# Optimization experiments

Hardware: AMD Instinct MI355X
Metric: run time of the kernel (lower is better)

Reference implementation:

```python
import jax, jax.numpy as jnp
import numpy as np

K = 20      # neighbors per node
D_T = 32    # timestep embedding dim

def _timestep_embedding(t, dim):
    half = dim // 2
    freqs = jnp.exp(-jnp.log(10000.0) * jnp.arange(half, dtype=jnp.float32) / (half - 1))
    args = t[:, None] * freqs[None, :]
    return jnp.concatenate([jnp.sin(args), jnp.cos(args)], axis=-1)

def _knn(pos, k):
    # pos: [N,3] -> (sources, targets): [N*k] edge index lists
    r2 = jnp.sum(pos * pos, axis=-1)
    d2 = r2[:, None] + r2[None, :] - 2.0 * (pos @ pos.T)   # [N,N] squared distances
    n = pos.shape[0]
    d2 = d2 + 1e10 * jnp.eye(n, dtype=pos.dtype)           # exclude self
    d2 = jax.lax.stop_gradient(d2)                         # indices only, no grad path
    _, idx = jax.lax.top_k(-d2, k)                         # [N,k]
    targets = jnp.repeat(jnp.arange(n), k)
    sources = idx.reshape(-1)
    return sources, targets

def _forward(z, t, conditioning, Wc1, bc1, Wc2, bc2, Wc3, bc3, We1, be1, We2, be2, Wn1, bn1, Wn2, bn2, alpha, beta):
    B, N, _ = z.shape
    pos, vel, massf = z[..., :3], z[..., 3:6], z[..., 6:]
    t = t * jnp.ones((B,), z.dtype)
    temb = _timestep_embedding(t, D_T)                     # [B,32]
    cond = jnp.concatenate([temb, conditioning], axis=1)   # [B,36]
    h = jax.nn.gelu(cond @ Wc1 + bc1)
    h = jax.nn.gelu(h @ Wc2 + bc2)
    cond = h @ Wc3 + bc3                                   # [B,36]
    fs = massf + cond[:, None, :]                          # scalar node feats [B,N,36]

    def single(pos_b, vel_b, fs_b):
        src, tgt = _knn(pos_b, K)
        rel = pos_b[src] - pos_b[tgt]                      # [E,3]
        r2 = jnp.sum(rel * rel, axis=-1, keepdims=True)
        vs, vt = vel_b[src], vel_b[tgt]
        # rotation-invariant edge features
        inv = jnp.concatenate([
            fs_b[src], fs_b[tgt], r2,
            jnp.sum(vs * vt, -1, keepdims=True),
            jnp.sum(vs * rel, -1, keepdims=True),
            jnp.sum(vt * rel, -1, keepdims=True),
        ], axis=-1)                                        # [E,76]
        e = jax.nn.gelu(inv @ We1 + be1) @ We2 + be2       # [E,4]
        logit, smsg, c_rel, c_vel = e[:, 0], e[:, 1], e[:, 2], e[:, 3]
        # segment softmax over incoming edges of each target node
        m = jax.ops.segment_max(logit, tgt, num_segments=N)
        a = jnp.exp(logit - m[tgt])
        denom = jax.ops.segment_sum(a, tgt, num_segments=N)
        w = a / denom[tgt]
        # equivariant vector messages, invariant scalar messages
        vmsg = w[:, None] * (c_rel[:, None] * rel + c_vel[:, None] * vs)
        vagg = jax.ops.segment_sum(vmsg, tgt, num_segments=N)              # [N,3]
        sagg = jax.ops.segment_sum(w * smsg, tgt, num_segments=N)[:, None]  # [N,1]
        hn = jax.nn.gelu(jnp.concatenate([fs_b, sagg], axis=-1) @ Wn1 + bn1)
        sout = hn @ Wn2 + bn2                              # [N,1] 0e output
        pos_out = pos_b + alpha * vagg                     # 1o
        feat_out = jnp.concatenate([beta * vagg, sout], axis=-1)  # 1o + 0e
        return jnp.concatenate([pos_out, feat_out], axis=-1)      # [N,7]

    h_all = jax.vmap(single)(pos, vel, fs)
    return z + h_all

def setup_inputs():
    key = jax.random.key(0)
    ks = jax.random.split(key, 10)
    B, N = 2, 8192
    d_cond = D_T + 4          # 36
    e_in = 2 * d_cond + 4     # 76
    e_hid, n_hid = 128, 64
    g = lambda i, shp: jax.random.normal(ks[i], shp, jnp.float32) * 0.05
    return {
        "z": jax.random.normal(ks[0], (B, N, 7), jnp.float32),
        "t": jax.random.uniform(ks[1], (B,), jnp.float32),
        "conditioning": jax.random.normal(ks[2], (B, 4), jnp.float32),
        "mask": jnp.ones((B, N), dtype=bool),
        "Wc1": g(3, (d_cond, 4 * d_cond)), "bc1": jnp.zeros((4 * d_cond,), jnp.float32),
        "Wc2": g(4, (4 * d_cond, 4 * d_cond)), "bc2": jnp.zeros((4 * d_cond,), jnp.float32),
        "Wc3": g(5, (4 * d_cond, d_cond)), "bc3": jnp.zeros((d_cond,), jnp.float32),
        "We1": g(6, (e_in, e_hid)), "be1": jnp.zeros((e_hid,), jnp.float32),
        "We2": g(7, (e_hid, 4)), "be2": jnp.zeros((4,), jnp.float32),
        "Wn1": g(8, (d_cond + 1, n_hid)), "bn1": jnp.zeros((n_hid,), jnp.float32),
        "Wn2": g(9, (n_hid, 1)), "bn2": jnp.zeros((1,), jnp.float32),
        "alpha": jnp.float32(0.1), "beta": jnp.float32(0.1),
    }

def reference(z, t, conditioning, mask, Wc1, bc1, Wc2, bc2, Wc3, bc3, We1, be1, We2, be2, Wn1, bn1, Wn2, bn2, alpha, beta):
    # mask is unused (module docstring: does not support masking)
    return _forward(z, t, conditioning, Wc1, bc1, Wc2, bc2, Wc3, bc3, We1, be1, We2, be2, Wn1, bn1, Wn2, bn2, alpha, beta)
```

## Files before the change

### kernel.cpp

```cpp
#include <hip/hip_runtime.h>
#include <math.h>

#define NB 8192
#define BATCH 2
#define KNN 20
#define BN (BATCH*NB)
#define NE (BN*KNN)
#define GT 16
#define NG 8
#define BIG 3.0e38f

__device__ __forceinline__ float gelu_f(float x){
    float x3 = x*x*x;
    float a = 0.7978845608028654f*(x + 0.044715f*x3);
    float e2 = __expf(2.0f*a);
    float th = 1.0f - __fdividef(2.0f, e2+1.0f);
    return 0.5f*x*(1.0f+th);
}

__global__ __launch_bounds__(256) void prepcond_kernel(const float* __restrict__ z,
        const float* __restrict__ t,
        const float* __restrict__ conditioning,
        const float* __restrict__ Wc1, const float* __restrict__ bc1,
        const float* __restrict__ Wc2, const float* __restrict__ bc2,
        const float* __restrict__ Wc3, const float* __restrict__ bc3,
        const float* __restrict__ We1, const float* __restrict__ be1,
        const float* __restrict__ We2,
        const float* __restrict__ Wn1, const float* __restrict__ bn1,
        float4* __restrict__ pos4, float4* __restrict__ vel4,
        float* __restrict__ consts, float* __restrict__ pack){
    int tid = threadIdx.x;
    int g = blockIdx.x*256 + tid;
    const float* zp = z + (size_t)g*7;
    float x = zp[0], y = zp[1], zz = zp[2];
    float r2 = x*x + y*y + zz*zz;
    pos4[g] = make_float4(x, y, zz, r2);
    vel4[g] = make_float4(zp[3], zp[4], zp[5], zp[6]);

    if (blockIdx.x >= BATCH) return;
    int b = blockIdx.x;
    __shared__ float ci[36];
    __shared__ float h1[144];
    __shared__ float h2[144];
    __shared__ float cnd[36];
    float tv = t[b];
    if (tid < 16){
        float f = expf(-9.210340371976184f * (float)tid / 15.0f);
        float a = tv*f;
        ci[tid]    = sinf(a);
        ci[16+tid] = cosf(a);
    }
    if (tid < 4) ci[32+tid] = conditioning[b*4+tid];
    __syncthreads();
    if (tid < 144){
        float acc = bc1[tid];
        #pragma unroll
        for (int c=0;c<36;c++) acc += ci[c]*Wc1[c*144+tid];
        h1[tid] = gelu_f(acc);
    }
    __syncthreads();
    if (tid < 144){
        float acc = bc2[tid];
        #pragma unroll 36
        for (int c=0;c<144;c++) acc += h1[c]*Wc2[c*144+tid];
        h2[tid] = gelu_f(acc);
    }
    __syncthreads();
    if (tid < 36){
        float acc = bc3[tid];
        #pragma unroll 36
        for (int c=0;c<144;c++) acc += h2[c]*Wc3[c*36+tid];
        cnd[tid] = acc;
    }
    __syncthreads();
    if (tid < 128){
        float accC = be1[tid], s1 = 0.f, s2 = 0.f;
        #pragma unroll
        for (int c=0;c<36;c++){
            float w1 = We1[c*128+tid];
            float w2 = We1[(36+c)*128+tid];
            accC += cnd[c]*(w1+w2);
            s1 += w1; s2 += w2;
        }
        consts[b*128+tid] = accC;
        pack[tid*12 + b] = accC;
        if (b==0){
            consts[256+tid] = s1; consts[384+tid] = s2;
            pack[tid*12+2] = s1;
            pack[tid*12+3] = s2;
            pack[tid*12+4] = We1[72*128+tid];
            pack[tid*12+5] = We1[73*128+tid];
            pack[tid*12+6] = We1[74*128+tid];
            pack[tid*12+7] = We1[75*128+tid];
            pack[tid*12+8]  = We2[tid*4+0];
            pack[tid*12+9]  = We2[tid*4+1];
            pack[tid*12+10] = We2[tid*4+2];
            pack[tid*12+11] = We2[tid*4+3];
        }
    }
    if (tid < 64){
        float accD = bn1[tid], t1 = 0.f;
        #pragma unroll
        for (int c=0;c<36;c++){
            float w = Wn1[c*64+tid];
            accD += cnd[c]*w;
            t1 += w;
        }
        consts[512 + b*64 + tid] = accD;
        if (b==0) consts[640+tid] = t1;
    }
}

__global__ __launch_bounds__(512, 4) void knn_kernel(const float4* __restrict__ pos4,
                                                     int* __restrict__ nbr){
    __shared__ float4 sPos[GT*64];
    __shared__ float2 sCand[32*64];
    int tid = threadIdx.x;
    int w = tid >> 6, lane = tid & 63;
    int n0g = blockIdx.x * 32;
    int b = n0g >> 13;
    int n0 = n0g & (NB-1);
    const float4* __restrict__ P = pos4 + b*NB;

    int nw = n0 + w*4;
    float nx[4], ny[4], nz[4], acc[4];
    #pragma unroll
    for (int k=0;k<4;k++){
        float4 p = P[nw+k];
        nx[k] = -2.0f*p.x; ny[k] = -2.0f*p.y; nz[k] = -2.0f*p.z;
        acc[k] = BIG;
    }
    int selfTile = n0 >> 6;
    int sl0 = (n0 & 63) + w*4;

    float4 pre0 = P[(w*2    )*64 + lane];
    float4 pre1 = P[(w*2 + 1)*64 + lane];
    for (int g=0; g<NG; ++g){
        __syncthreads();
        sPos[(w*2    )*64 + lane] = pre0;
        sPos[(w*2 + 1)*64 + lane] = pre1;
        if (g+1 < NG){
            pre0 = P[((g+1)*GT + w*2    )*64 + lane];
            pre1 = P[((g+1)*GT + w*2 + 1)*64 + lane];
        }
        __syncthreads();
        int tbase = g*GT;
        #pragma unroll
        for (int t=0;t<GT;t++){
            float4 q = sPos[t*64 + lane];
            if (tbase + t != selfTile){
                #pragma unroll
                for (int k=0;k<4;k++){
                    float d2 = fmaf(nx[k],q.x, fmaf(ny[k],q.y, fmaf(nz[k],q.z, q.w)));
                    acc[k] = fminf(acc[k], d2);
                }
            } else {
                #pragma unroll
                for (int k=0;k<4;k++){
                    float d2 = fmaf(nx[k],q.x, fmaf(ny[k],q.y, fmaf(nz[k],q.z, q.w)));
                    if (lane == sl0 + k) d2 = BIG;
                    acc[k] = fminf(acc[k], d2);
                }
            }
        }
    }

    float T[4];
    #pragma unroll
    for (int k=0;k<4;k++){
        float v = acc[k];
        #pragma unroll
        for (int K=2; K<=64; K<<=1){
            #pragma unroll
            for (int j=K>>1; j>0; j>>=1){
                float o = __shfl_xor(v, j);
                bool keepmin = (((lane & j) == 0) == ((lane & K) == 0));
                float mn = fminf(v,o), mx = fmaxf(v,o);
                v = keepmin ? mn : mx;
            }
        }
        T[k] = __shfl(v, 19);
    }

    int cnt[4];
    #pragma unroll
    for (int k=0;k<4;k++) cnt[k] = 0;
    unsigned long long lt = (1ull << lane) - 1ull;

    pre0 = P[(w*2    )*64 + lane];
    pre1 = P[(w*2 + 1)*64 + lane];
    for (int g=0; g<NG; ++g){
        __syncthreads();
        sPos[(w*2    )*64 + lane] = pre0;
        sPos[(w*2 + 1)*64 + lane] = pre1;
        if (g+1 < NG){
            pre0 = P[((g+1)*GT + w*2    )*64 + lane];
            pre1 = P[((g+1)*GT + w*2 + 1)*64 + lane];
        }
        __syncthreads();
        int tbase = g*GT;
        #pragma unroll 4
        for (int t=0;t<GT;t++){
            int tile = tbase + t;
            float4 q = sPos[t*64 + lane];
            int j = (tile<<6) + lane;
            bool selft = (tile == selfTile);
            #pragma unroll
            for (int k=0;k<4;k++){
                float d2 = fmaf(nx[k],q.x, fmaf(ny[k],q.y, fmaf(nz[k],q.z, q.w)));
                bool hit = (d2 <= T[k]);
                if (selft && (lane == sl0 + k)) hit = false;
                unsigned long long m = __ballot(hit);
                if (m){
                    if (hit){
                        int off = cnt[k] + (int)__popcll(m & lt);
                        if (off < 64)
                            sCand[(w*4+k)*64 + off] = make_float2(d2, __int_as_float(j));
                    }
                    cnt[k] += (int)__popcll(m);
                }
            }
        }
    }

    #pragma unroll
    for (int k=0;k<4;k++){
        int m = cnt[k]; if (m > 64) m = 64;
        float d; int idx;
        if (lane < m){
            float2 e = sCand[(w*4+k)*64 + lane];
            d = e.x; idx = __float_as_int(e.y);
        } else { d = BIG; idx = 0x7f000000 + lane; }
        #pragma unroll
        for (int K=2; K<=64; K<<=1){
            #pragma unroll
            for (int j=K>>1; j>0; j>>=1){
                float od = __shfl_xor(d, j);
                int   oi = __shfl_xor(idx, j);
                bool pless = (od < d) || (od == d && oi < idx);
                bool keepmin = (((lane & j) == 0) == ((lane & K) == 0));
                if (pless == keepmin){ d = od; idx = oi; }
            }
        }
        if (lane < KNN) nbr[(size_t)(n0g + w*4 + k)*KNN + lane] = idx;
    }
}

__global__ __launch_bounds__(320) void edgenode_kernel(const float4* __restrict__ pos4,
        const float4* __restrict__ vel4,
        const int* __restrict__ nbr,
        const float* __restrict__ pack,
        const float* __restrict__ consts,
        const float* __restrict__ Wn1,
        const float* __restrict__ Wn2,
        const float* __restrict__ be2,
        const float* __restrict__ bn2,
        const float* __restrict__ alpha_p,
        const float* __restrict__ beta_p,
        const float* __restrict__ z,
        float* __restrict__ out){
    __shared__ float4 sP[384];
    __shared__ float sLg[320], sSm[320], sUx[320], sUy[320], sUz[320];
    __shared__ float sD[64], sT1[64], sW36[64], sWo[64];
    __shared__ float sMf[16];
    __shared__ float4 sAgg[16];
    __shared__ float sPart[320];

    int tid = threadIdx.x;
    bool bb = (blockIdx.x >= 512);
    for (int k=tid; k<384; k+=320) sP[k] = ((const float4*)pack)[k];
    if (tid < 64){
        sD[tid]   = consts[512 + (bb?64:0) + tid];
        sT1[tid]  = consts[640+tid];
        sW36[tid] = Wn1[36*64+tid];
        sWo[tid]  = Wn2[tid];
    }

    int e = blockIdx.x*320 + tid;
    int i = e / KNN;
    int ln = tid / KNN;
    int r  = tid - ln*KNN;
    int bbase = bb ? NB : 0;
    int s = nbr[e];
    float4 ps = pos4[bbase + s], pt = pos4[i];
    float4 vs = vel4[bbase + s], vt = vel4[i];
    if (r == 0) sMf[ln] = vt.w;

    float rx = ps.x - pt.x, ry = ps.y - pt.y, rz = ps.z - pt.z;
    float r2  = rx*rx + ry*ry + rz*rz;
    float vv  = vs.x*vt.x + vs.y*vt.y + vs.z*vt.z;
    float vsr = vs.x*rx + vs.y*ry + vs.z*rz;
    float vtr = vt.x*rx + vt.y*ry + vt.z*rz;
    float mfs = vs.w, mft = vt.w;
    __syncthreads();

    float a0 = be2[0], a1 = be2[1], a2 = be2[2], a3 = be2[3];
    #pragma unroll 4
    for (int h=0; h<128; h++){
        float4 A  = sP[h*3];
        float4 Bv = sP[h*3+1];
        float4 C  = sP[h*3+2];
        float base = bb ? A.y : A.x;
        float x = base + mfs*A.z + mft*A.w + r2*Bv.x + vv*Bv.y + vsr*Bv.z + vtr*Bv.w;
        float gx = gelu_f(x);
        a0 += gx*C.x; a1 += gx*C.y; a2 += gx*C.z; a3 += gx*C.w;
    }
    sLg[tid] = a0;
    sSm[tid] = a1;
    sUx[tid] = a2*rx + a3*vs.x;
    sUy[tid] = a2*ry + a3*vs.y;
    sUz[tid] = a2*rz + a3*vs.z;
    __syncthreads();

    if (tid < 16){
        int base = tid*KNN;
        float m = -BIG;
        #pragma unroll
        for (int q=0;q<KNN;q++) m = fmaxf(m, sLg[base+q]);
        float den=0.f, wx=0.f, wy=0.f, wz=0.f, wsm=0.f;
        #pragma unroll
        for (int q=0;q<KNN;q++){
            float a = __expf(sLg[base+q]-m);
            den += a;
            wsm += a*sSm[base+q];
            wx  += a*sUx[base+q];
            wy  += a*sUy[base+q];
            wz  += a*sUz[base+q];
        }
        float inv = __fdividef(1.0f, den);
        sAgg[tid] = make_float4(wx*inv, wy*inv, wz*inv, wsm*inv);
    }
    __syncthreads();

    {
        float mf = sMf[ln];
        float sg = sAgg[ln].w;
        float part = 0.f;
        #pragma unroll
        for (int h=r; h<64; h+=KNN){
            float x = sD[h] + mf*sT1[h] + sg*sW36[h];
            part += gelu_f(x)*sWo[h];
        }
        sPart[tid] = part;
    }
    __syncthreads();

    if (tid < 16){
        float sout = bn2[0];
        #pragma unroll
        for (int q=0;q<KNN;q++) sout += sPart[tid*KNN+q];
        int node = blockIdx.x*16 + tid;
        float alpha = alpha_p[0], beta = beta_p[0];
        float4 ag = sAgg[tid];
        const float* zp = z + (size_t)node*7;
        float* op = out + (size_t)node*7;
        op[0] = zp[0]*2.0f + alpha*ag.x;
        op[1] = zp[1]*2.0f + alpha*ag.y;
        op[2] = zp[2]*2.0f + alpha*ag.z;
        op[3] = zp[3] + beta*ag.x;
        op[4] = zp[4] + beta*ag.y;
        op[5] = zp[5] + beta*ag.z;
        op[6] = zp[6] + sout;
    }
}

extern "C" void kernel_launch(void* const* d_in, const int* in_sizes, int n_in,
                              void* d_out, int out_size, void* d_ws, size_t ws_size,
                              hipStream_t stream) {
    const float* z    = (const float*)d_in[0];
    const float* t    = (const float*)d_in[1];
    const float* cond = (const float*)d_in[2];
    const float* Wc1  = (const float*)d_in[4];
    const float* bc1  = (const float*)d_in[5];
    const float* Wc2  = (const float*)d_in[6];
    const float* bc2  = (const float*)d_in[7];
    const float* Wc3  = (const float*)d_in[8];
    const float* bc3  = (const float*)d_in[9];
    const float* We1  = (const float*)d_in[10];
    const float* be1  = (const float*)d_in[11];
    const float* We2  = (const float*)d_in[12];
    const float* be2  = (const float*)d_in[13];
    const float* Wn1  = (const float*)d_in[14];
    const float* bn1  = (const float*)d_in[15];
    const float* Wn2  = (const float*)d_in[16];
    const float* bn2  = (const float*)d_in[17];
    const float* alp  = (const float*)d_in[18];
    const float* bet  = (const float*)d_in[19];
    float* out = (float*)d_out;

    char* ws = (char*)d_ws;
    float4* pos4   = (float4*)(ws);
    float4* vel4   = (float4*)(ws + 262144);
    float*  consts = (float*)(ws + 524288);
    float*  pack   = (float*)(ws + 528384);
    int*    nbr    = (int*)(ws + 534528);

    prepcond_kernel<<<dim3(BN/256), dim3(256), 0, stream>>>(z, t, cond,
        Wc1, bc1, Wc2, bc2, Wc3, bc3, We1, be1, We2, Wn1, bn1,
        pos4, vel4, consts, pack);
    knn_kernel<<<dim3(BN/32), dim3(512), 0, stream>>>(pos4, nbr);
    edgenode_kernel<<<dim3(BN/16), dim3(320), 0, stream>>>(pos4, vel4, nbr, pack, consts,
        Wn1, Wn2, be2, bn2, alp, bet, z, out);
}
```

Before: 201.5 us.

## Process two edges per thread in edgenode kernel and simplify GELU formula

Each thread in the edge/node kernel now handles two edges (32 nodes per block instead of 16), so each shared-memory weight load in the 128-wide hidden loop is reused for two edges. The block count halves and the batch split moves to block 256. GELU's tanh approximation is rewritten algebraically as x/(1+exp(-2a)), which saves a few instructions per evaluation. The trade-off is higher register pressure, more shared memory per block and fewer blocks.

```diff
diff --git a/kernel.cpp b/kernel.cpp
--- a/kernel.cpp
+++ b/kernel.cpp
@@ -11,11 +11,10 @@
 #define BIG 3.0e38f
 
 __device__ __forceinline__ float gelu_f(float x){
-    float x3 = x*x*x;
-    float a = 0.7978845608028654f*(x + 0.044715f*x3);
-    float e2 = __expf(2.0f*a);
-    float th = 1.0f - __fdividef(2.0f, e2+1.0f);
-    return 0.5f*x*(1.0f+th);
+    float t = x*x;
+    float m = x*fmaf(t, -0.0713548163f, -1.5957691216f);
+    float e = __expf(m);
+    return __fdividef(x, 1.0f + e);
 }
 
 __global__ __launch_bounds__(256) void prepcond_kernel(const float* __restrict__ z,
@@ -260,14 +259,14 @@
         const float* __restrict__ z,
         float* __restrict__ out){
     __shared__ float4 sP[384];
-    __shared__ float sLg[320], sSm[320], sUx[320], sUy[320], sUz[320];
+    __shared__ float sLg[640], sSm[640], sUx[640], sUy[640], sUz[640];
     __shared__ float sD[64], sT1[64], sW36[64], sWo[64];
-    __shared__ float sMf[16];
-    __shared__ float4 sAgg[16];
-    __shared__ float sPart[320];
+    __shared__ float sMf[32];
+    __shared__ float4 sAgg[32];
+    __shared__ float sPart[640];
 
     int tid = threadIdx.x;
-    bool bb = (blockIdx.x >= 512);
+    bool bb = (blockIdx.x >= 256);
     for (int k=tid; k<384; k+=320) sP[k] = ((const float4*)pack)[k];
     if (tid < 64){
         sD[tid]   = consts[512 + (bb?64:0) + tid];
@@ -276,43 +275,58 @@
         sWo[tid]  = Wn2[tid];
     }
 
-    int e = blockIdx.x*320 + tid;
-    int i = e / KNN;
-    int ln = tid / KNN;
-    int r  = tid - ln*KNN;
+    int e0 = blockIdx.x*640 + tid;
+    int e1 = e0 + 320;
+    int i0 = e0 / KNN;
+    int i1 = i0 + 16;
+    int ln0 = tid / KNN;
+    int r  = tid - ln0*KNN;
     int bbase = bb ? NB : 0;
-    int s = nbr[e];
-    float4 ps = pos4[bbase + s], pt = pos4[i];
-    float4 vs = vel4[bbase + s], vt = vel4[i];
-    if (r == 0) sMf[ln] = vt.w;
-
-    float rx = ps.x - pt.x, ry = ps.y - pt.y, rz = ps.z - pt.z;
-    float r2  = rx*rx + ry*ry + rz*rz;
-    float vv  = vs.x*vt.x + vs.y*vt.y + vs.z*vt.z;
-    float vsr = vs.x*rx + vs.y*ry + vs.z*rz;
-    float vtr = vt.x*rx + vt.y*ry + vt.z*rz;
-    float mfs = vs.w, mft = vt.w;
-    __syncthreads();
-
-    float a0 = be2[0], a1 = be2[1], a2 = be2[2], a3 = be2[3];
-    #pragma unroll 4
+    int s0 = nbr[e0], s1 = nbr[e1];
+    float4 ps0 = pos4[bbase + s0], pt0 = pos4[i0];
+    float4 vs0 = vel4[bbase + s0], vt0 = vel4[i0];
+    float4 ps1 = pos4[bbase + s1], pt1 = pos4[i1];
+    float4 vs1 = vel4[bbase + s1], vt1 = vel4[i1];
+    if (r == 0){ sMf[ln0] = vt0.w; sMf[ln0+16] = vt1.w; }
+
+    float rx0 = ps0.x - pt0.x, ry0 = ps0.y - pt0.y, rz0 = ps0.z - pt0.z;
+    float r20  = rx0*rx0 + ry0*ry0 + rz0*rz0;
+    float vv0  = vs0.x*vt0.x + vs0.y*vt0.y + vs0.z*vt0.z;
+    float vsr0 = vs0.x*rx0 + vs0.y*ry0 + vs0.z*rz0;
+    float vtr0 = vt0.x*rx0 + vt0.y*ry0 + vt0.z*rz0;
+    float mfs0 = vs0.w, mft0 = vt0.w;
+
+    float rx1 = ps1.x - pt1.x, ry1 = ps1.y - pt1.y, rz1 = ps1.z - pt1.z;
+    float r21  = rx1*rx1 + ry1*ry1 + rz1*rz1;
+    float vv1  = vs1.x*vt1.x + vs1.y*vt1.y + vs1.z*vt1.z;
+    float vsr1 = vs1.x*rx1 + vs1.y*ry1 + vs1.z*rz1;
+    float vtr1 = vt1.x*rx1 + vt1.y*ry1 + vt1.z*rz1;
+    float mfs1 = vs1.w, mft1 = vt1.w;
+    __syncthreads();
+
+    float a00 = be2[0], a10 = be2[1], a20 = be2[2], a30 = be2[3];
+    float a01 = a00, a11 = a10, a21 = a20, a31 = a30;
+    #pragma unroll 2
     for (int h=0; h<128; h++){
         float4 A  = sP[h*3];
         float4 Bv = sP[h*3+1];
         float4 C  = sP[h*3+2];
         float base = bb ? A.y : A.x;
-        float x = base + mfs*A.z + mft*A.w + r2*Bv.x + vv*Bv.y + vsr*Bv.z + vtr*Bv.w;
-        float gx = gelu_f(x);
-        a0 += gx*C.x; a1 += gx*C.y; a2 += gx*C.z; a3 += gx*C.w;
-    }
-    sLg[tid] = a0;
-    sSm[tid] = a1;
-    sUx[tid] = a2*rx + a3*vs.x;
-    sUy[tid] = a2*ry + a3*vs.y;
-    sUz[tid] = a2*rz + a3*vs.z;
-    __syncthreads();
-
-    if (tid < 16){
+        float x0 = base + mfs0*A.z + mft0*A.w + r20*Bv.x + vv0*Bv.y + vsr0*Bv.z + vtr0*Bv.w;
+        float x1 = base + mfs1*A.z + mft1*A.w + r21*Bv.x + vv1*Bv.y + vsr1*Bv.z + vtr1*Bv.w;
+        float g0 = gelu_f(x0);
+        float g1 = gelu_f(x1);
+        a00 += g0*C.x; a10 += g0*C.y; a20 += g0*C.z; a30 += g0*C.w;
+        a01 += g1*C.x; a11 += g1*C.y; a21 += g1*C.z; a31 += g1*C.w;
+    }
+    sLg[tid]     = a00;  sLg[tid+320] = a01;
+    sSm[tid]     = a10;  sSm[tid+320] = a11;
+    sUx[tid]     = a20*rx0 + a30*vs0.x;  sUx[tid+320] = a21*rx1 + a31*vs1.x;
+    sUy[tid]     = a20*ry0 + a30*vs0.y;  sUy[tid+320] = a21*ry1 + a31*vs1.y;
+    sUz[tid]     = a20*rz0 + a30*vs0.z;  sUz[tid+320] = a21*rz1 + a31*vs1.z;
+    __syncthreads();
+
+    if (tid < 32){
         int base = tid*KNN;
         float m = -BIG;
         #pragma unroll
@@ -333,23 +347,26 @@
     __syncthreads();
 
     {
-        float mf = sMf[ln];
-        float sg = sAgg[ln].w;
-        float part = 0.f;
+        float mf0 = sMf[ln0],     sg0 = sAgg[ln0].w;
+        float mf1 = sMf[ln0+16],  sg1 = sAgg[ln0+16].w;
+        float p0 = 0.f, p1 = 0.f;
         #pragma unroll
         for (int h=r; h<64; h+=KNN){
-            float x = sD[h] + mf*sT1[h] + sg*sW36[h];
-            part += gelu_f(x)*sWo[h];
-        }
-        sPart[tid] = part;
-    }
-    __syncthreads();
-
-    if (tid < 16){
+            float x0 = sD[h] + mf0*sT1[h] + sg0*sW36[h];
+            float x1 = sD[h] + mf1*sT1[h] + sg1*sW36[h];
+            p0 += gelu_f(x0)*sWo[h];
+            p1 += gelu_f(x1)*sWo[h];
+        }
+        sPart[tid]     = p0;
+        sPart[tid+320] = p1;
+    }
+    __syncthreads();
+
+    if (tid < 32){
         float sout = bn2[0];
         #pragma unroll
         for (int q=0;q<KNN;q++) sout += sPart[tid*KNN+q];
-        int node = blockIdx.x*16 + tid;
+        int node = blockIdx.x*32 + tid;
         float alpha = alpha_p[0], beta = beta_p[0];
         float4 ag = sAgg[tid];
         const float* zp = z + (size_t)node*7;
@@ -399,6 +416,6 @@
         Wc1, bc1, Wc2, bc2, Wc3, bc3, We1, be1, We2, Wn1, bn1,
         pos4, vel4, consts, pack);
     knn_kernel<<<dim3(BN/32), dim3(512), 0, stream>>>(pos4, nbr);
-    edgenode_kernel<<<dim3(BN/16), dim3(320), 0, stream>>>(pos4, vel4, nbr, pack, consts,
+    edgenode_kernel<<<dim3(NE/640), dim3(320), 0, stream>>>(pos4, vel4, nbr, pack, consts,
         Wn1, Wn2, be2, bn2, alp, bet, z, out);
 }
```

Result: no change. 205.2 us (+1.9%).
